# Optimization experiments

Measured on AMD Instinct MI355X. Metric: run time of the kernel, lower is better.

Reference implementation:

```python
import jax, jax.numpy as jnp
import numpy as np

B, A, N, FIN, H, HEADS, OUT = 32, 64, 121, 12, 128, 4, 256
NL = 2          # transformer encoder layers
LEVELS = 4      # complete ternary tree: N = (3**(LEVELS+1)-1)//2 = 121
EPS = 1e-5


def setup_inputs() -> dict:
    key = jax.random.key(0)
    ks = jax.random.split(key, 10)
    s = 0.02
    # adjacency: complete ternary tree, local node indices, rows [parent, child, branch]
    child = np.arange(1, N)
    parent = (child - 1) // 3
    branch = (child - 1) % 3
    adj = np.stack([parent, child, branch], -1).astype(np.int32)  # (N-1, 3)
    adjacency = jnp.asarray(np.broadcast_to(adj, (B, A, N - 1, 3)).copy())
    perm = jax.random.permutation(ks[0], N)  # torch.randperm(n_nodes) equivalent
    forest = jax.random.normal(ks[1], (B, A, N, FIN), jnp.float32)
    p = lambda k, shape: s * jax.random.normal(k, shape, jnp.float32)
    return dict(
        forest=forest, adjacency=adjacency, perm=perm,
        w_in=p(ks[2], (H, FIN)), b_in=jnp.zeros((H,), jnp.float32),
        qkv_w=p(ks[3], (NL, 3 * H, H)), qkv_b=jnp.zeros((NL, 3 * H), jnp.float32),
        proj_w=p(ks[4], (NL, H, H)), proj_b=jnp.zeros((NL, H), jnp.float32),
        ff1_w=p(ks[5], (NL, H, H)), ff1_b=jnp.zeros((NL, H), jnp.float32),
        ff2_w=p(ks[6], (NL, H, H)), ff2_b=jnp.zeros((NL, H), jnp.float32),
        ln1_g=jnp.ones((NL, H), jnp.float32), ln1_b=jnp.zeros((NL, H), jnp.float32),
        ln2_g=jnp.ones((NL, H), jnp.float32), ln2_b=jnp.zeros((NL, H), jnp.float32),
        w_out=p(ks[7], (OUT, N * H)), b_out=jnp.zeros((OUT,), jnp.float32),
        lnf_g=jnp.ones((OUT,), jnp.float32), lnf_b=jnp.zeros((OUT,), jnp.float32))


def _ln(x, g, b):
    m = x.mean(-1, keepdims=True)
    v = ((x - m) ** 2).mean(-1, keepdims=True)  # biased var, as torch LayerNorm
    return (x - m) * jax.lax.rsqrt(v + EPS) * g + b


def _tree_pe(adjacency):
    """Level-parallel tree positional encoding: pe[child] = pe[parent] with
    bit (depth*3 + branch) set to 1 (depth 0 = first level below root)."""
    parent = adjacency[..., 0]
    branch = adjacency[..., 2]
    pe = jnp.zeros((B, A, N, H), jnp.float32)
    for l in range(1, LEVELS + 1):
        s0 = (3 ** l - 1) // 2          # first node index at level l
        e0 = (3 ** (l + 1) - 1) // 2    # one past last node at level l
        pa = parent[..., s0 - 1:e0 - 1]             # (B, A, n_l) parent local idx
        br = branch[..., s0 - 1:e0 - 1]             # (B, A, n_l) branch 0/1/2
        ppe = jnp.take_along_axis(pe, pa[..., None], axis=2)  # gather parent PE
        bits = jax.nn.one_hot((l - 1) * 3 + br, H, dtype=jnp.float32)
        pe = pe.at[:, :, s0:e0, :].set(ppe + bits)
    return pe


def _mha(x, wqkv, bqkv, wo, bo):
    S = x.shape[0]
    hd = H // HEADS
    qkv = x @ wqkv.T + bqkv
    q, k, v = [t.reshape(S, N, HEADS, hd) for t in jnp.split(qkv, 3, axis=-1)]
    logits = jnp.einsum('bqhd,bkhd->bhqk', q, k) / float(np.sqrt(hd))
    o = jnp.einsum('bhqk,bkhd->bqhd', jax.nn.softmax(logits, -1), v)
    return o.reshape(S, N, H) @ wo.T + bo


def _forward(forest, adjacency, perm, w_in, b_in, qkv_w, qkv_b, proj_w, proj_b,
             ff1_w, ff1_b, ff2_w, ff2_b, ln1_g, ln1_b, ln2_g, ln2_b,
             w_out, b_out, lnf_g, lnf_b):
    x = forest @ w_in.T + b_in + _tree_pe(adjacency)        # (B, A, N, H)
    x = x.reshape(B * A, N, H)[:, perm]                      # token shuffle
    for i in range(NL):  # post-norm encoder layers, relu FFN, dropout=0
        x = _ln(x + _mha(x, qkv_w[i], qkv_b[i], proj_w[i], proj_b[i]), ln1_g[i], ln1_b[i])
        h = jnp.maximum(x @ ff1_w[i].T + ff1_b[i], 0.0)
        x = _ln(x + h @ ff2_w[i].T + ff2_b[i], ln2_g[i], ln2_b[i])
    y = x.reshape(B * A, N * H) @ w_out.T + b_out
    return _ln(y.reshape(B, A, OUT), lnf_g, lnf_b)


def reference(forest, adjacency, perm, w_in, b_in, qkv_w, qkv_b, proj_w, proj_b,
              ff1_w, ff1_b, ff2_w, ff2_b, ln1_g, ln1_b, ln2_g, ln2_b,
              w_out, b_out, lnf_g, lnf_b):
    return _forward(forest, adjacency, perm, w_in, b_in, qkv_w, qkv_b, proj_w, proj_b,
                    ff1_w, ff1_b, ff2_w, ff2_b, ln1_g, ln1_b, ln2_g, ln2_b,
                    w_out, b_out, lnf_g, lnf_b)
```

## Files before the change

kernel.cpp:

```cpp
#include <hip/hip_runtime.h>


typedef unsigned short u16;
typedef __attribute__((ext_vector_type(8))) short bf16x8;
typedef __attribute__((ext_vector_type(4))) float f32x4;
typedef __attribute__((ext_vector_type(4))) unsigned int u32x4;
typedef __attribute__((ext_vector_type(2))) unsigned int u32x2;

#define NTOK 121
#define HD 128
#define S_TOT 2048
#define EPSF 1e-5f

__device__ inline u16 f2bf(float f) {
  unsigned u = __float_as_uint(f);
  return (u16)((u + 0x7FFFu + ((u >> 16) & 1u)) >> 16);
}
__device__ inline float bf2f(u16 h) { return __uint_as_float(((unsigned)h) << 16); }
__device__ inline float bfu32lo(unsigned u) { return __uint_as_float(u << 16); }
__device__ inline float bfu32hi(unsigned u) { return __uint_as_float(u & 0xffff0000u); }

__device__ inline f32x4 mfma16(bf16x8 a, bf16x8 b, f32x4 c) {
  return __builtin_amdgcn_mfma_f32_16x16x32_bf16(a, b, c, 0, 0, 0);
}

__device__ inline unsigned cvt_pk_bf16(float lo, float hi) {
  unsigned r;
  asm("v_cvt_pk_bf16_f32 %0, %1, %2" : "=v"(r) : "v"(lo), "v"(hi));
  return r;
}

__device__ inline f32x4 vmax4(f32x4 a, f32x4 b) {
  f32x4 r;
  r[0] = fmaxf(a[0], b[0]); r[1] = fmaxf(a[1], b[1]);
  r[2] = fmaxf(a[2], b[2]); r[3] = fmaxf(a[3], b[3]);
  return r;
}

__device__ inline void stage16(const void* g, void* l) {
  __builtin_amdgcn_global_load_lds((__attribute__((address_space(1))) void*)g,
                                   (__attribute__((address_space(3))) void*)l,
                                   16, 0, 0);
}

__device__ inline void quad_repack(unsigned pkA, unsigned pkB, int quad,
                                   unsigned& mlo, unsigned& mhi) {
  unsigned y = (quad < 2) ? pkA : pkB;
  unsigned z = (quad < 2) ? pkB : pkA;
  unsigned a16 = (unsigned)__shfl_xor((int)y, 16);
  unsigned a32 = (unsigned)__shfl_xor((int)z, 32);
  unsigned a48 = (unsigned)__shfl_xor((int)z, 48);
  mlo = (quad == 0) ? y   : (quad == 1) ? a48 : (quad == 2) ? a32 : a16;
  mhi = (quad == 0) ? a16 : (quad == 1) ? a32 : (quad == 2) ? a48 : y;
}

__global__ __launch_bounds__(256) void convw_kernel(
    const float* __restrict__ qkvw, const float* __restrict__ projw,
    const float* __restrict__ ff1w, const float* __restrict__ ff2w,
    const float* __restrict__ wout, u16* __restrict__ dst) {
  int i = blockIdx.x * 256 + threadIdx.x;
  float v;
  if (i < 98304) v = qkvw[i];
  else if (i < 131072) v = projw[i - 98304];
  else if (i < 163840) v = ff1w[i - 131072];
  else if (i < 196608) v = ff2w[i - 163840];
  else v = wout[i - 196608];
  dst[i] = f2bf(v);
}

__global__ __launch_bounds__(256) void inproj_kernel(
    const float* __restrict__ forest, const int* __restrict__ adj,
    const int* __restrict__ perm, const float* __restrict__ WIN,
    const float* __restrict__ BIN, u16* __restrict__ X) {
  __shared__ float wf[128 * 12];
  __shared__ float fr[121 * 12];
  __shared__ float pe[121 * 12];
  __shared__ int pm[121];
  int s = blockIdx.x, tid = threadIdx.x;
  const float* fg = forest + (size_t)s * (NTOK * 12);
  const int* ag = adj + (size_t)s * (120 * 3);
  for (int i = tid; i < 128 * 12; i += 256) wf[i] = WIN[i];
  for (int i = tid; i < 121 * 12; i += 256) { fr[i] = fg[i]; pe[i] = 0.f; }
  if (tid < 121) pm[tid] = perm[tid];
  __syncthreads();
  if (tid > 0 && tid < 121) {
    int n = tid;
    int l = (n <= 3) ? 1 : (n <= 12) ? 2 : (n <= 39) ? 3 : 4;
    int cur = n;
    while (cur > 0) {
      int par = ag[(cur - 1) * 3];
      int br = ag[(cur - 1) * 3 + 2];
      pe[n * 12 + (l - 1) * 3 + br] = 1.f;
      cur = par; l--;
    }
  }
  __syncthreads();
  int h = tid & 127;
  for (int base = 0; base < 121; base += 2) {
    int i = base + (tid >> 7);
    if (i < 121) {
      int node = pm[i];
      float v = BIN[h];
#pragma unroll
      for (int k = 0; k < 12; ++k) v += fr[node * 12 + k] * wf[h * 12 + k];
      if (h < 12) v += pe[node * 12 + h];
      X[(size_t)s * (NTOK * HD) + i * HD + h] = f2bf(v);
    }
  }
}

__global__ __launch_bounds__(256, 3) void attn_kernel(
    const u16* __restrict__ X, u16* __restrict__ O,
    const u16* __restrict__ WQKV, const float* __restrict__ QKVB, int layer) {
  __shared__ u16 lds[8192];
  __shared__ u16 xl[15872];
  int tid = threadIdx.x;
  int wave = tid >> 6, lane = tid & 63, l16 = lane & 15, quad = lane >> 4;
  int seq = blockIdx.x >> 2;
  int head = blockIdx.x & 3;
  u16* Kh = lds;
  u16* Vh = lds + 4096;
  const u16* Xs = X + (size_t)seq * (NTOK * HD);
  const f32x4 fz = {0.f, 0.f, 0.f, 0.f};
  const int wbase = layer * 384 + head * 32;
  const u16* WQ = WQKV + (size_t)wbase * HD;
  const u16* WK = WQKV + (size_t)(wbase + 128) * HD;
  const u16* WV = WQKV + (size_t)(wbase + 256) * HD;

  {
    const char* Xb = (const char*)Xs;
#pragma unroll
    for (int j = 0; j < 8; ++j) {
      int i = wave * 8 + j;
      if (i < 31) {
        int n = i * 64 + lane;
        int r = n >> 4, c = n & 15;
        int rc = r > 120 ? 120 : r;
        stage16(Xb + rc * 256 + ((c ^ (r & 7)) << 4), (void*)(xl + i * 512));
      }
    }
  }
  bf16x8 wqf[2][4], wkf[2][4], wvf[2][4];
#pragma unroll
  for (int nt = 0; nt < 2; ++nt)
#pragma unroll
    for (int k = 0; k < 4; ++k) {
      size_t off = (size_t)(nt * 16 + l16) * HD + k * 32 + quad * 8;
      wqf[nt][k] = *(const bf16x8*)(WQ + off);
      wkf[nt][k] = *(const bf16x8*)(WK + off);
      wvf[nt][k] = *(const bf16x8*)(WV + off);
    }
  float kb2[2], vb2[2];
#pragma unroll
  for (int nt = 0; nt < 2; ++nt) {
    kb2[nt] = QKVB[wbase + 128 + nt * 16 + l16];
    vb2[nt] = QKVB[wbase + 256 + nt * 16 + l16];
  }
  const float scl = 0.17677669529663687f * 1.4426950408889634f;
  float qbias[2][4];
#pragma unroll
  for (int nt = 0; nt < 2; ++nt)
#pragma unroll
    for (int r = 0; r < 4; ++r)
      qbias[nt][r] = QKVB[wbase + nt * 16 + quad * 4 + r];
  asm volatile("s_waitcnt vmcnt(0)" ::: "memory");
  __syncthreads();

#pragma unroll 1
  for (int mt = 0; mt < 2; ++mt) {
    int tb = wave * 32 + mt * 16;
    int arow = tb + l16; if (arow > 120) arow = 120;
    bf16x8 a[4];
#pragma unroll
    for (int k = 0; k < 4; ++k)
      a[k] = *(const bf16x8*)(xl + arow * 128 + (((k * 4 + quad) ^ (arow & 7)) << 3));
#pragma unroll
    for (int nt = 0; nt < 2; ++nt) {
      f32x4 kacc = fz, vacc = fz;
      __builtin_amdgcn_s_setprio(1);
#pragma unroll
      for (int k = 0; k < 4; ++k) {
        kacc = mfma16(a[k], wkf[nt][k], kacc);
        vacc = mfma16(a[k], wvf[nt][k], vacc);
      }
      __builtin_amdgcn_s_setprio(0);
      int d = nt * 16 + l16;
      int kc = nt * 2 + (l16 >> 3);
#pragma unroll
      for (int r = 0; r < 4; ++r) {
        int t = tb + quad * 4 + r;
        Kh[t * 32 + ((kc ^ (t & 3)) << 3) + (l16 & 7)] = f2bf(kacc[r] + kb2[nt]);
      }
      float vv[4];
#pragma unroll
      for (int r = 0; r < 4; ++r) {
        int t = tb + quad * 4 + r;
        vv[r] = (t < NTOK) ? (vacc[r] + vb2[nt]) : 0.f;
      }
      u32x2 vp = { cvt_pk_bf16(vv[0], vv[1]), cvt_pk_bf16(vv[2], vv[3]) };
      *(u32x2*)(Vh + d * 128 + ((((tb >> 3) + (quad >> 1)) ^ l16) << 3) + (quad & 1) * 4) = vp;
    }
  }
  __syncthreads();

#pragma unroll 1
  for (int qmt = 0; qmt < 2; ++qmt) {
    int qb = wave * 32 + qmt * 16;
    int qrow = qb + l16;
    int qrowc = qrow > 120 ? 120 : qrow;
    bf16x8 xb[4];
#pragma unroll
    for (int k = 0; k < 4; ++k)
      xb[k] = *(const bf16x8*)(xl + qrowc * 128 + (((k * 4 + quad) ^ (qrowc & 7)) << 3));
    f32x4 qv[2];
    __builtin_amdgcn_s_setprio(1);
#pragma unroll
    for (int nt = 0; nt < 2; ++nt) {
      f32x4 acc = fz;
#pragma unroll
      for (int k = 0; k < 4; ++k) acc = mfma16(wqf[nt][k], xb[k], acc);
      qv[nt] = acc;
    }
    __builtin_amdgcn_s_setprio(0);
    unsigned qpk[2][2];
#pragma unroll
    for (int nt = 0; nt < 2; ++nt)
#pragma unroll
      for (int r2 = 0; r2 < 2; ++r2)
        qpk[nt][r2] = cvt_pk_bf16((qv[nt][2 * r2] + qbias[nt][2 * r2]) * scl,
                                  (qv[nt][2 * r2 + 1] + qbias[nt][2 * r2 + 1]) * scl);
    u32x4 qu;
#pragma unroll
    for (int r2 = 0; r2 < 2; ++r2) {
      unsigned mlo, mhi;
      quad_repack(qpk[0][r2], qpk[1][r2], quad, mlo, mhi);
      qu[r2] = mlo; qu[2 + r2] = mhi;
    }
    bf16x8 qfrag = __builtin_bit_cast(bf16x8, qu);
    f32x4 lg[8];
    __builtin_amdgcn_s_setprio(1);
#pragma unroll
    for (int nt = 0; nt < 8; ++nt) {
      bf16x8 ka = *(const bf16x8*)(Kh + (nt * 16 + l16) * 32 + ((quad ^ (l16 & 3)) << 3));
      lg[nt] = mfma16(ka, qfrag, fz);
    }
    __builtin_amdgcn_s_setprio(0);
    f32x4 t0 = vmax4(vmax4(lg[0], lg[1]), vmax4(lg[2], lg[3]));
    f32x4 t1 = vmax4(vmax4(lg[4], lg[5]), vmax4(lg[6], lg[7]));
    f32x4 tm = vmax4(t0, t1);
    float mx = fmaxf(fmaxf(tm[0], tm[1]), fmaxf(tm[2], tm[3]));
    mx = fmaxf(mx, __shfl_xor(mx, 16));
    mx = fmaxf(mx, __shfl_xor(mx, 32));
#pragma unroll
    for (int nt = 0; nt < 8; ++nt)
#pragma unroll
      for (int r = 0; r < 4; ++r) {
        float ev = __builtin_amdgcn_exp2f(lg[nt][r] - mx);
        if (nt == 7 && (quad * 4 + r > 8)) ev = 0.f;
        lg[nt][r] = ev;
      }
    f32x4 s4 = (lg[0] + lg[1]) + (lg[2] + lg[3]) + ((lg[4] + lg[5]) + (lg[6] + lg[7]));
    float sum = (s4[0] + s4[1]) + (s4[2] + s4[3]);
    sum += __shfl_xor(sum, 16);
    sum += __shfl_xor(sum, 32);
    float rinv = __builtin_amdgcn_rcpf(sum);
    unsigned pk[8][2];
#pragma unroll
    for (int nt = 0; nt < 8; ++nt)
#pragma unroll
      for (int r2 = 0; r2 < 2; ++r2)
        pk[nt][r2] = cvt_pk_bf16(lg[nt][2 * r2], lg[nt][2 * r2 + 1]);
    f32x4 oacc[2] = {fz, fz};
#pragma unroll
    for (int s = 0; s < 4; ++s) {
      u32x4 pu;
#pragma unroll
      for (int r2 = 0; r2 < 2; ++r2) {
        unsigned mlo, mhi;
        quad_repack(pk[2 * s][r2], pk[2 * s + 1][r2], quad, mlo, mhi);
        pu[r2] = mlo; pu[2 + r2] = mhi;
      }
      bf16x8 pfrag = __builtin_bit_cast(bf16x8, pu);
      __builtin_amdgcn_s_setprio(1);
#pragma unroll
      for (int mt = 0; mt < 2; ++mt) {
        bf16x8 va = *(const bf16x8*)(Vh + (mt * 16 + l16) * 128 + (((s * 4 + quad) ^ l16) << 3));
        oacc[mt] = mfma16(va, pfrag, oacc[mt]);
      }
      __builtin_amdgcn_s_setprio(0);
    }
    if (qrow < NTOK) {
      u16* Op = O + (size_t)seq * (NTOK * HD) + (size_t)qrow * HD + head * 32;
#pragma unroll
      for (int mt = 0; mt < 2; ++mt) {
        u32x2 w = { cvt_pk_bf16(oacc[mt][0] * rinv, oacc[mt][1] * rinv),
                    cvt_pk_bf16(oacc[mt][2] * rinv, oacc[mt][3] * rinv) };
        *(u32x2*)(Op + mt * 16 + quad * 4) = w;
      }
    }
  }
}

__global__ __launch_bounds__(256, 2) void blockln_kernel(
    u16* __restrict__ X, const u16* __restrict__ O,
    const u16* __restrict__ WP, const float* __restrict__ PB,
    const u16* __restrict__ W1, const float* __restrict__ B1,
    const u16* __restrict__ W2, const float* __restrict__ B2,
    const float* __restrict__ G1, const float* __restrict__ Bt1,
    const float* __restrict__ G2, const float* __restrict__ Bt2, int layer) {
  __shared__ u16 as_[128 * 128];
  __shared__ u16 xr[128 * 128];
  __shared__ float part[1024];
  int r0 = blockIdx.x * 128, tid = threadIdx.x;
  int wave = tid >> 6, lane = tid & 63, l16 = lane & 15, quad = lane >> 4;
  const f32x4 fz = {0.f, 0.f, 0.f, 0.f};
  const int Lb = layer * 128;
  const int ch0 = wave * 32;
  const int ch8b = wave * 4 + (quad >> 1);

  {
    const char* Ob = (const char*)(O + (size_t)r0 * HD);
    const char* Xb = (const char*)(X + (size_t)r0 * HD);
#pragma unroll
    for (int j = 0; j < 8; ++j) {
      int n = wave * 512 + j * 64 + lane;
      int r = n >> 4, c = n & 15;
      int gsrc = r * 256 + ((c ^ (r & 7)) << 4);
      stage16(Ob + gsrc, (void*)(as_ + (wave * 512 + j * 64) * 8));
      stage16(Xb + gsrc, (void*)(xr + (wave * 512 + j * 64) * 8));
    }
  }
  bf16x8 wpf[2][4], w1f[2][4], w2f[2][4];
#pragma unroll
  for (int g = 0; g < 2; ++g)
#pragma unroll
    for (int k = 0; k < 4; ++k) {
      size_t off = (size_t)(Lb + ch0 + g * 16 + l16) * HD + k * 32 + quad * 8;
      wpf[g][k] = *(const bf16x8*)(WP + off);
      w1f[g][k] = *(const bf16x8*)(W1 + off);
      w2f[g][k] = *(const bf16x8*)(W2 + off);
    }
  asm volatile("s_waitcnt vmcnt(0)" ::: "memory");
  __syncthreads();

  f32x4 acc[2][8];
#pragma unroll
  for (int mt = 0; mt < 8; ++mt) {
    int tok = mt * 16 + l16;
    bf16x8 of[4];
#pragma unroll
    for (int k = 0; k < 4; ++k)
      of[k] = *(const bf16x8*)(as_ + tok * 128 + (((k * 4 + quad) ^ (tok & 7)) << 3));
    __builtin_amdgcn_s_setprio(1);
#pragma unroll
    for (int g = 0; g < 2; ++g) {
      f32x4 a = fz;
#pragma unroll
      for (int k = 0; k < 4; ++k) a = mfma16(wpf[g][k], of[k], a);
      acc[g][mt] = a;
    }
    __builtin_amdgcn_s_setprio(0);
    float sum = 0.f, ssq = 0.f;
#pragma unroll
    for (int g = 0; g < 2; ++g) {
      float4 pb4 = *(const float4*)(PB + Lb + ch0 + g * 16 + quad * 4);
      int sl = (ch8b + g * 2) ^ (tok & 7);
      u32x2 xw = *(const u32x2*)(xr + tok * 128 + (sl << 3) + (quad & 1) * 4);
      acc[g][mt][0] += pb4.x + bfu32lo(xw[0]);
      acc[g][mt][1] += pb4.y + bfu32hi(xw[0]);
      acc[g][mt][2] += pb4.z + bfu32lo(xw[1]);
      acc[g][mt][3] += pb4.w + bfu32hi(xw[1]);
#pragma unroll
      for (int r = 0; r < 4; ++r) { sum += acc[g][mt][r]; ssq += acc[g][mt][r] * acc[g][mt][r]; }
    }
    sum += __shfl_xor(sum, 16); ssq += __shfl_xor(ssq, 16);
    sum += __shfl_xor(sum, 32); ssq += __shfl_xor(ssq, 32);
    if (quad == 0) *(float2*)(part + ((mt * 4 + wave) * 16 + l16) * 2) = make_float2(sum, ssq);
  }
  __syncthreads();

#pragma unroll
  for (int mt = 0; mt < 8; ++mt) {
    int tok = mt * 16 + l16;
    float sum = 0.f, ssq = 0.f;
#pragma unroll
    for (int ww = 0; ww < 4; ++ww) {
      float2 p = *(const float2*)(part + ((mt * 4 + ww) * 16 + l16) * 2);
      sum += p.x; ssq += p.y;
    }
    float mean = sum * (1.f / 128.f);
    float rstd = rsqrtf(ssq * (1.f / 128.f) - mean * mean + EPSF);
#pragma unroll
    for (int g = 0; g < 2; ++g) {
      float4 g4 = *(const float4*)(G1 + Lb + ch0 + g * 16 + quad * 4);
      float4 b4 = *(const float4*)(Bt1 + Lb + ch0 + g * 16 + quad * 4);
      u32x2 wv = { cvt_pk_bf16((acc[g][mt][0] - mean) * rstd * g4.x + b4.x,
                               (acc[g][mt][1] - mean) * rstd * g4.y + b4.y),
                   cvt_pk_bf16((acc[g][mt][2] - mean) * rstd * g4.z + b4.z,
                               (acc[g][mt][3] - mean) * rstd * g4.w + b4.w) };
      int sl = (ch8b + g * 2) ^ (tok & 7);
      *(u32x2*)(as_ + tok * 128 + (sl << 3) + (quad & 1) * 4) = wv;
    }
  }
  __syncthreads();

#pragma unroll
  for (int mt = 0; mt < 8; ++mt) {
    int tok = mt * 16 + l16;
    bf16x8 af[4];
#pragma unroll
    for (int k = 0; k < 4; ++k)
      af[k] = *(const bf16x8*)(as_ + tok * 128 + (((k * 4 + quad) ^ (tok & 7)) << 3));
    __builtin_amdgcn_s_setprio(1);
#pragma unroll
    for (int g = 0; g < 2; ++g) {
      f32x4 a = fz;
#pragma unroll
      for (int k = 0; k < 4; ++k) a = mfma16(w1f[g][k], af[k], a);
      float4 b14 = *(const float4*)(B1 + Lb + ch0 + g * 16 + quad * 4);
      u32x2 wv = { cvt_pk_bf16(fmaxf(a[0] + b14.x, 0.f), fmaxf(a[1] + b14.y, 0.f)),
                   cvt_pk_bf16(fmaxf(a[2] + b14.z, 0.f), fmaxf(a[3] + b14.w, 0.f)) };
      int sl = (ch8b + g * 2) ^ (tok & 7);
      *(u32x2*)(xr + tok * 128 + (sl << 3) + (quad & 1) * 4) = wv;
    }
    __builtin_amdgcn_s_setprio(0);
  }
  __syncthreads();

#pragma unroll
  for (int mt = 0; mt < 8; ++mt) {
    int tok = mt * 16 + l16;
    bf16x8 hf[4];
#pragma unroll
    for (int k = 0; k < 4; ++k)
      hf[k] = *(const bf16x8*)(xr + tok * 128 + (((k * 4 + quad) ^ (tok & 7)) << 3));
    __builtin_amdgcn_s_setprio(1);
#pragma unroll
    for (int g = 0; g < 2; ++g) {
      f32x4 a = fz;
#pragma unroll
      for (int k = 0; k < 4; ++k) a = mfma16(w2f[g][k], hf[k], a);
      acc[g][mt] = a;
    }
    __builtin_amdgcn_s_setprio(0);
    float sum = 0.f, ssq = 0.f;
#pragma unroll
    for (int g = 0; g < 2; ++g) {
      float4 b24 = *(const float4*)(B2 + Lb + ch0 + g * 16 + quad * 4);
      int sl = (ch8b + g * 2) ^ (tok & 7);
      u32x2 lw = *(const u32x2*)(as_ + tok * 128 + (sl << 3) + (quad & 1) * 4);
      acc[g][mt][0] += b24.x + bfu32lo(lw[0]);
      acc[g][mt][1] += b24.y + bfu32hi(lw[0]);
      acc[g][mt][2] += b24.z + bfu32lo(lw[1]);
      acc[g][mt][3] += b24.w + bfu32hi(lw[1]);
#pragma unroll
      for (int r = 0; r < 4; ++r) { sum += acc[g][mt][r]; ssq += acc[g][mt][r] * acc[g][mt][r]; }
    }
    sum += __shfl_xor(sum, 16); ssq += __shfl_xor(ssq, 16);
    sum += __shfl_xor(sum, 32); ssq += __shfl_xor(ssq, 32);
    if (quad == 0) *(float2*)(part + ((mt * 4 + wave) * 16 + l16) * 2) = make_float2(sum, ssq);
  }
  __syncthreads();

#pragma unroll
  for (int mt = 0; mt < 8; ++mt) {
    int tok = mt * 16 + l16;
    float sum = 0.f, ssq = 0.f;
#pragma unroll
    for (int ww = 0; ww < 4; ++ww) {
      float2 p = *(const float2*)(part + ((mt * 4 + ww) * 16 + l16) * 2);
      sum += p.x; ssq += p.y;
    }
    float mean = sum * (1.f / 128.f);
    float rstd = rsqrtf(ssq * (1.f / 128.f) - mean * mean + EPSF);
    u16* Xp = X + (size_t)(r0 + tok) * HD + ch0;
#pragma unroll
    for (int g = 0; g < 2; ++g) {
      float4 g4 = *(const float4*)(G2 + Lb + ch0 + g * 16 + quad * 4);
      float4 b4 = *(const float4*)(Bt2 + Lb + ch0 + g * 16 + quad * 4);
      u32x2 wv = { cvt_pk_bf16((acc[g][mt][0] - mean) * rstd * g4.x + b4.x,
                               (acc[g][mt][1] - mean) * rstd * g4.y + b4.y),
                   cvt_pk_bf16((acc[g][mt][2] - mean) * rstd * g4.z + b4.z,
                               (acc[g][mt][3] - mean) * rstd * g4.w + b4.w) };
      *(u32x2*)(Xp + g * 16 + quad * 4) = wv;
    }
  }
}

__global__ __launch_bounds__(256, 2) void outgemm_kernel(
    const u16* __restrict__ X, const u16* __restrict__ WO, float* __restrict__ PART) {
  __shared__ u16 as_[64 * 136];
  int mtile = blockIdx.x, j = blockIdx.y;
  int tid = threadIdx.x, wave = tid >> 6, lane = tid & 63, l16 = lane & 15, quad = lane >> 4;
  int s0 = mtile * 64;
  int k0 = (j * 484) / 16, k1 = ((j + 1) * 484) / 16;
  const f32x4 fz = {0.f, 0.f, 0.f, 0.f};
  f32x4 acc[4][4];
  for (int a = 0; a < 4; ++a) for (int b = 0; b < 4; ++b) acc[a][b] = fz;
  for (int kb = k0; kb < k1; kb += 4) {
    int nst = (k1 - kb < 4) ? (k1 - kb) : 4;
    __syncthreads();
    int chunks = 64 * 4 * nst;
    for (int c = tid; c < chunks; c += 256) {
      int row = c / (4 * nst), g = c % (4 * nst);
      *(uint4*)(as_ + row * 136 + g * 8) =
          *(const uint4*)(X + (size_t)(s0 + row) * 15488 + kb * 32 + g * 8);
    }
    __syncthreads();
    for (int kk = 0; kk < nst; ++kk) {
      bf16x8 af[4];
#pragma unroll
      for (int mt = 0; mt < 4; ++mt)
        af[mt] = *(const bf16x8*)(as_ + (mt * 16 + l16) * 136 + kk * 32 + quad * 8);
#pragma unroll
      for (int n = 0; n < 4; ++n) {
        int nt = wave * 4 + n;
        bf16x8 bf = *(const bf16x8*)(WO + (size_t)(nt * 16 + l16) * 15488 +
                                     (size_t)(kb + kk) * 32 + quad * 8);
#pragma unroll
        for (int mt = 0; mt < 4; ++mt) acc[mt][n] = mfma16(af[mt], bf, acc[mt][n]);
      }
    }
  }
  for (int mt = 0; mt < 4; ++mt)
    for (int n = 0; n < 4; ++n) {
      int nt = wave * 4 + n;
#pragma unroll
      for (int r = 0; r < 4; ++r) {
        int row = s0 + mt * 16 + quad * 4 + r;
        PART[((size_t)j * 2048 + row) * 256 + nt * 16 + l16] = acc[mt][n][r];
      }
    }
}

__global__ __launch_bounds__(256) void lnf_kernel(
    const float* __restrict__ PART, const float* __restrict__ BO,
    const float* __restrict__ G, const float* __restrict__ Bt, float* __restrict__ OUT) {
  int s = blockIdx.x * 4 + (threadIdx.x >> 6);
  int lane = threadIdx.x & 63;
  float v[4], sum = 0.f, ssq = 0.f;
#pragma unroll
  for (int i = 0; i < 4; ++i) {
    int c = lane + i * 64;
    float t = BO[c];
    for (int jj = 0; jj < 16; ++jj) t += PART[((size_t)jj * 2048 + s) * 256 + c];
    v[i] = t; sum += t; ssq += t * t;
  }
  for (int m = 1; m <= 32; m <<= 1) { sum += __shfl_xor(sum, m, 64); ssq += __shfl_xor(ssq, m, 64); }
  float mean = sum * (1.f / 256.f);
  float var = ssq * (1.f / 256.f) - mean * mean;
  float rstd = rsqrtf(var + EPSF);
#pragma unroll
  for (int i = 0; i < 4; ++i) {
    int c = lane + i * 64;
    OUT[(size_t)s * 256 + c] = (v[i] - mean) * rstd * G[c] + Bt[c];
  }
}

extern "C" void kernel_launch(void* const* d_in, const int* in_sizes, int n_in,
                              void* d_out, int out_size, void* d_ws, size_t ws_size,
                              hipStream_t stream) {
  const float* forest = (const float*)d_in[0];
  const int* adj      = (const int*)d_in[1];
  const int* perm     = (const int*)d_in[2];
  const float* w_in   = (const float*)d_in[3];
  const float* b_in   = (const float*)d_in[4];
  const float* qkv_w  = (const float*)d_in[5];
  const float* qkv_b  = (const float*)d_in[6];
  const float* proj_w = (const float*)d_in[7];
  const float* proj_b = (const float*)d_in[8];
  const float* ff1_w  = (const float*)d_in[9];
  const float* ff1_b  = (const float*)d_in[10];
  const float* ff2_w  = (const float*)d_in[11];
  const float* ff2_b  = (const float*)d_in[12];
  const float* ln1_g  = (const float*)d_in[13];
  const float* ln1_b  = (const float*)d_in[14];
  const float* ln2_g  = (const float*)d_in[15];
  const float* ln2_b  = (const float*)d_in[16];
  const float* w_out  = (const float*)d_in[17];
  const float* b_out  = (const float*)d_in[18];
  const float* lnf_g  = (const float*)d_in[19];
  const float* lnf_b  = (const float*)d_in[20];

  char* ws = (char*)d_ws;
  u16* WB = (u16*)ws;
  u16* X  = (u16*)(ws + 8323072);
  u16* O  = (u16*)(ws + 8323072 + 63438848);
  float* PART = (float*)(ws + 8323072 + 2 * (size_t)63438848);

  u16* WQKV  = WB;
  u16* WPROJ = WB + 98304;
  u16* WFF1  = WB + 131072;
  u16* WFF2  = WB + 163840;
  u16* WOUT  = WB + 196608;

  convw_kernel<<<16256, 256, 0, stream>>>(qkv_w, proj_w, ff1_w, ff2_w, w_out, WB);
  inproj_kernel<<<2048, 256, 0, stream>>>(forest, adj, perm, w_in, b_in, X);
  for (int layer = 0; layer < 2; ++layer) {
    attn_kernel<<<8192, 256, 0, stream>>>(X, O, WQKV, qkv_b, layer);
    blockln_kernel<<<1936, 256, 0, stream>>>(X, O, WPROJ, proj_b, WFF1, ff1_b,
                                             WFF2, ff2_b, ln1_g, ln1_b, ln2_g, ln2_b, layer);
  }
  outgemm_kernel<<<dim3(32, 16), 256, 0, stream>>>(X, WOUT, PART);
  lnf_kernel<<<512, 256, 0, stream>>>(PART, b_out, lnf_g, lnf_b, (float*)d_out);
}
```

Measured before the change: 610.7 us.

## Process two attention heads per block to reuse staged sequence tile

Each attention block now handles two heads of one sequence, not one, so the grid is halved. The sequence's X tile is staged into LDS once and reused for both heads. This halves the global X reads and the staging overhead. In exchange each block does serial work for two heads, with a reload of the per-head weights and an extra barrier between them, and there are fewer blocks to hide latency.

```diff
diff --git a/kernel.cpp b/kernel.cpp
--- a/kernel.cpp
+++ b/kernel.cpp
@@ -109,6 +109,26 @@
   }
 }
 
+#define LOADW()                                                              \
+  do {                                                                       \
+    const u16* WQ = WQKV + (size_t)wbase * HD;                               \
+    const u16* WK = WQKV + (size_t)(wbase + 128) * HD;                       \
+    const u16* WV = WQKV + (size_t)(wbase + 256) * HD;                       \
+    _Pragma("unroll") for (int nt = 0; nt < 2; ++nt)                         \
+        _Pragma("unroll") for (int k = 0; k < 4; ++k) {                      \
+      size_t off = (size_t)(nt * 16 + l16) * HD + k * 32 + quad * 8;         \
+      wqf[nt][k] = *(const bf16x8*)(WQ + off);                               \
+      wkf[nt][k] = *(const bf16x8*)(WK + off);                               \
+      wvf[nt][k] = *(const bf16x8*)(WV + off);                               \
+    }                                                                        \
+    _Pragma("unroll") for (int nt = 0; nt < 2; ++nt) {                       \
+      kb2[nt] = QKVB[wbase + 128 + nt * 16 + l16];                           \
+      vb2[nt] = QKVB[wbase + 256 + nt * 16 + l16];                           \
+      _Pragma("unroll") for (int r = 0; r < 4; ++r)                          \
+          qbias[nt][r] = QKVB[wbase + nt * 16 + quad * 4 + r];               \
+    }                                                                        \
+  } while (0)
+
 __global__ __launch_bounds__(256, 3) void attn_kernel(
     const u16* __restrict__ X, u16* __restrict__ O,
     const u16* __restrict__ WQKV, const float* __restrict__ QKVB, int layer) {
@@ -116,16 +136,13 @@
   __shared__ u16 xl[15872];
   int tid = threadIdx.x;
   int wave = tid >> 6, lane = tid & 63, l16 = lane & 15, quad = lane >> 4;
-  int seq = blockIdx.x >> 2;
-  int head = blockIdx.x & 3;
+  int seq = blockIdx.x >> 1;
+  int hb = (blockIdx.x & 1) << 1;
   u16* Kh = lds;
   u16* Vh = lds + 4096;
   const u16* Xs = X + (size_t)seq * (NTOK * HD);
   const f32x4 fz = {0.f, 0.f, 0.f, 0.f};
-  const int wbase = layer * 384 + head * 32;
-  const u16* WQ = WQKV + (size_t)wbase * HD;
-  const u16* WK = WQKV + (size_t)(wbase + 128) * HD;
-  const u16* WV = WQKV + (size_t)(wbase + 256) * HD;
+  const float scl = 0.17677669529663687f * 1.4426950408889634f;
 
   {
     const char* Xb = (const char*)Xs;
@@ -141,163 +158,154 @@
     }
   }
   bf16x8 wqf[2][4], wkf[2][4], wvf[2][4];
-#pragma unroll
-  for (int nt = 0; nt < 2; ++nt)
-#pragma unroll
-    for (int k = 0; k < 4; ++k) {
-      size_t off = (size_t)(nt * 16 + l16) * HD + k * 32 + quad * 8;
-      wqf[nt][k] = *(const bf16x8*)(WQ + off);
-      wkf[nt][k] = *(const bf16x8*)(WK + off);
-      wvf[nt][k] = *(const bf16x8*)(WV + off);
-    }
-  float kb2[2], vb2[2];
-#pragma unroll
-  for (int nt = 0; nt < 2; ++nt) {
-    kb2[nt] = QKVB[wbase + 128 + nt * 16 + l16];
-    vb2[nt] = QKVB[wbase + 256 + nt * 16 + l16];
-  }
-  const float scl = 0.17677669529663687f * 1.4426950408889634f;
-  float qbias[2][4];
-#pragma unroll
-  for (int nt = 0; nt < 2; ++nt)
-#pragma unroll
-    for (int r = 0; r < 4; ++r)
-      qbias[nt][r] = QKVB[wbase + nt * 16 + quad * 4 + r];
+  float kb2[2], vb2[2], qbias[2][4];
+  int wbase = layer * 384 + hb * 32;
+  LOADW();
   asm volatile("s_waitcnt vmcnt(0)" ::: "memory");
   __syncthreads();
 
 #pragma unroll 1
-  for (int mt = 0; mt < 2; ++mt) {
-    int tb = wave * 32 + mt * 16;
-    int arow = tb + l16; if (arow > 120) arow = 120;
-    bf16x8 a[4];
-#pragma unroll
-    for (int k = 0; k < 4; ++k)
-      a[k] = *(const bf16x8*)(xl + arow * 128 + (((k * 4 + quad) ^ (arow & 7)) << 3));
-#pragma unroll
-    for (int nt = 0; nt < 2; ++nt) {
-      f32x4 kacc = fz, vacc = fz;
+  for (int hp = 0; hp < 2; ++hp) {
+    if (hp) {
+      wbase = layer * 384 + (hb + 1) * 32;
+      LOADW();
+    }
+    int head = hb + hp;
+
+#pragma unroll 1
+    for (int mt = 0; mt < 2; ++mt) {
+      int tb = wave * 32 + mt * 16;
+      int arow = tb + l16; if (arow > 120) arow = 120;
+      bf16x8 a[4];
+#pragma unroll
+      for (int k = 0; k < 4; ++k)
+        a[k] = *(const bf16x8*)(xl + arow * 128 + (((k * 4 + quad) ^ (arow & 7)) << 3));
+#pragma unroll
+      for (int nt = 0; nt < 2; ++nt) {
+        f32x4 kacc = fz, vacc = fz;
+        __builtin_amdgcn_s_setprio(1);
+#pragma unroll
+        for (int k = 0; k < 4; ++k) {
+          kacc = mfma16(a[k], wkf[nt][k], kacc);
+          vacc = mfma16(a[k], wvf[nt][k], vacc);
+        }
+        __builtin_amdgcn_s_setprio(0);
+        int d = nt * 16 + l16;
+        int kc = nt * 2 + (l16 >> 3);
+#pragma unroll
+        for (int r = 0; r < 4; ++r) {
+          int t = tb + quad * 4 + r;
+          Kh[t * 32 + ((kc ^ (t & 3)) << 3) + (l16 & 7)] = f2bf(kacc[r] + kb2[nt]);
+        }
+        float vv[4];
+#pragma unroll
+        for (int r = 0; r < 4; ++r) {
+          int t = tb + quad * 4 + r;
+          vv[r] = (t < NTOK) ? (vacc[r] + vb2[nt]) : 0.f;
+        }
+        u32x2 vp = { cvt_pk_bf16(vv[0], vv[1]), cvt_pk_bf16(vv[2], vv[3]) };
+        *(u32x2*)(Vh + d * 128 + ((((tb >> 3) + (quad >> 1)) ^ l16) << 3) + (quad & 1) * 4) = vp;
+      }
+    }
+    __syncthreads();
+
+#pragma unroll 1
+    for (int qmt = 0; qmt < 2; ++qmt) {
+      int qb = wave * 32 + qmt * 16;
+      int qrow = qb + l16;
+      int qrowc = qrow > 120 ? 120 : qrow;
+      bf16x8 xb[4];
+#pragma unroll
+      for (int k = 0; k < 4; ++k)
+        xb[k] = *(const bf16x8*)(xl + qrowc * 128 + (((k * 4 + quad) ^ (qrowc & 7)) << 3));
+      f32x4 qv[2];
       __builtin_amdgcn_s_setprio(1);
 #pragma unroll
-      for (int k = 0; k < 4; ++k) {
-        kacc = mfma16(a[k], wkf[nt][k], kacc);
-        vacc = mfma16(a[k], wvf[nt][k], vacc);
+      for (int nt = 0; nt < 2; ++nt) {
+        f32x4 acc = fz;
+#pragma unroll
+        for (int k = 0; k < 4; ++k) acc = mfma16(wqf[nt][k], xb[k], acc);
+        qv[nt] = acc;
       }
       __builtin_amdgcn_s_setprio(0);
-      int d = nt * 16 + l16;
-      int kc = nt * 2 + (l16 >> 3);
-#pragma unroll
-      for (int r = 0; r < 4; ++r) {
-        int t = tb + quad * 4 + r;
-        Kh[t * 32 + ((kc ^ (t & 3)) << 3) + (l16 & 7)] = f2bf(kacc[r] + kb2[nt]);
-      }
-      float vv[4];
-#pragma unroll
-      for (int r = 0; r < 4; ++r) {
-        int t = tb + quad * 4 + r;
-        vv[r] = (t < NTOK) ? (vacc[r] + vb2[nt]) : 0.f;
-      }
-      u32x2 vp = { cvt_pk_bf16(vv[0], vv[1]), cvt_pk_bf16(vv[2], vv[3]) };
-      *(u32x2*)(Vh + d * 128 + ((((tb >> 3) + (quad >> 1)) ^ l16) << 3) + (quad & 1) * 4) = vp;
-    }
-  }
-  __syncthreads();
-
-#pragma unroll 1
-  for (int qmt = 0; qmt < 2; ++qmt) {
-    int qb = wave * 32 + qmt * 16;
-    int qrow = qb + l16;
-    int qrowc = qrow > 120 ? 120 : qrow;
-    bf16x8 xb[4];
-#pragma unroll
-    for (int k = 0; k < 4; ++k)
-      xb[k] = *(const bf16x8*)(xl + qrowc * 128 + (((k * 4 + quad) ^ (qrowc & 7)) << 3));
-    f32x4 qv[2];
-    __builtin_amdgcn_s_setprio(1);
-#pragma unroll
-    for (int nt = 0; nt < 2; ++nt) {
-      f32x4 acc = fz;
-#pragma unroll
-      for (int k = 0; k < 4; ++k) acc = mfma16(wqf[nt][k], xb[k], acc);
-      qv[nt] = acc;
-    }
-    __builtin_amdgcn_s_setprio(0);
-    unsigned qpk[2][2];
-#pragma unroll
-    for (int nt = 0; nt < 2; ++nt)
-#pragma unroll
-      for (int r2 = 0; r2 < 2; ++r2)
-        qpk[nt][r2] = cvt_pk_bf16((qv[nt][2 * r2] + qbias[nt][2 * r2]) * scl,
-                                  (qv[nt][2 * r2 + 1] + qbias[nt][2 * r2 + 1]) * scl);
-    u32x4 qu;
-#pragma unroll
-    for (int r2 = 0; r2 < 2; ++r2) {
-      unsigned mlo, mhi;
-      quad_repack(qpk[0][r2], qpk[1][r2], quad, mlo, mhi);
-      qu[r2] = mlo; qu[2 + r2] = mhi;
-    }
-    bf16x8 qfrag = __builtin_bit_cast(bf16x8, qu);
-    f32x4 lg[8];
-    __builtin_amdgcn_s_setprio(1);
-#pragma unroll
-    for (int nt = 0; nt < 8; ++nt) {
-      bf16x8 ka = *(const bf16x8*)(Kh + (nt * 16 + l16) * 32 + ((quad ^ (l16 & 3)) << 3));
-      lg[nt] = mfma16(ka, qfrag, fz);
-    }
-    __builtin_amdgcn_s_setprio(0);
-    f32x4 t0 = vmax4(vmax4(lg[0], lg[1]), vmax4(lg[2], lg[3]));
-    f32x4 t1 = vmax4(vmax4(lg[4], lg[5]), vmax4(lg[6], lg[7]));
-    f32x4 tm = vmax4(t0, t1);
-    float mx = fmaxf(fmaxf(tm[0], tm[1]), fmaxf(tm[2], tm[3]));
-    mx = fmaxf(mx, __shfl_xor(mx, 16));
-    mx = fmaxf(mx, __shfl_xor(mx, 32));
-#pragma unroll
-    for (int nt = 0; nt < 8; ++nt)
-#pragma unroll
-      for (int r = 0; r < 4; ++r) {
-        float ev = __builtin_amdgcn_exp2f(lg[nt][r] - mx);
-        if (nt == 7 && (quad * 4 + r > 8)) ev = 0.f;
-        lg[nt][r] = ev;
-      }
-    f32x4 s4 = (lg[0] + lg[1]) + (lg[2] + lg[3]) + ((lg[4] + lg[5]) + (lg[6] + lg[7]));
-    float sum = (s4[0] + s4[1]) + (s4[2] + s4[3]);
-    sum += __shfl_xor(sum, 16);
-    sum += __shfl_xor(sum, 32);
-    float rinv = __builtin_amdgcn_rcpf(sum);
-    unsigned pk[8][2];
-#pragma unroll
-    for (int nt = 0; nt < 8; ++nt)
-#pragma unroll
-      for (int r2 = 0; r2 < 2; ++r2)
-        pk[nt][r2] = cvt_pk_bf16(lg[nt][2 * r2], lg[nt][2 * r2 + 1]);
-    f32x4 oacc[2] = {fz, fz};
-#pragma unroll
-    for (int s = 0; s < 4; ++s) {
-      u32x4 pu;
+      unsigned qpk[2][2];
+#pragma unroll
+      for (int nt = 0; nt < 2; ++nt)
+#pragma unroll
+        for (int r2 = 0; r2 < 2; ++r2)
+          qpk[nt][r2] = cvt_pk_bf16((qv[nt][2 * r2] + qbias[nt][2 * r2]) * scl,
+                                    (qv[nt][2 * r2 + 1] + qbias[nt][2 * r2 + 1]) * scl);
+      u32x4 qu;
 #pragma unroll
       for (int r2 = 0; r2 < 2; ++r2) {
         unsigned mlo, mhi;
-        quad_repack(pk[2 * s][r2], pk[2 * s + 1][r2], quad, mlo, mhi);
-        pu[r2] = mlo; pu[2 + r2] = mhi;
-      }
-      bf16x8 pfrag = __builtin_bit_cast(bf16x8, pu);
+        quad_repack(qpk[0][r2], qpk[1][r2], quad, mlo, mhi);
+        qu[r2] = mlo; qu[2 + r2] = mhi;
+      }
+      bf16x8 qfrag = __builtin_bit_cast(bf16x8, qu);
+      f32x4 lg[8];
       __builtin_amdgcn_s_setprio(1);
 #pragma unroll
-      for (int mt = 0; mt < 2; ++mt) {
-        bf16x8 va = *(const bf16x8*)(Vh + (mt * 16 + l16) * 128 + (((s * 4 + quad) ^ l16) << 3));
-        oacc[mt] = mfma16(va, pfrag, oacc[mt]);
+      for (int nt = 0; nt < 8; ++nt) {
+        bf16x8 ka = *(const bf16x8*)(Kh + (nt * 16 + l16) * 32 + ((quad ^ (l16 & 3)) << 3));
+        lg[nt] = mfma16(ka, qfrag, fz);
       }
       __builtin_amdgcn_s_setprio(0);
-    }
-    if (qrow < NTOK) {
-      u16* Op = O + (size_t)seq * (NTOK * HD) + (size_t)qrow * HD + head * 32;
-#pragma unroll
-      for (int mt = 0; mt < 2; ++mt) {
-        u32x2 w = { cvt_pk_bf16(oacc[mt][0] * rinv, oacc[mt][1] * rinv),
-                    cvt_pk_bf16(oacc[mt][2] * rinv, oacc[mt][3] * rinv) };
-        *(u32x2*)(Op + mt * 16 + quad * 4) = w;
-      }
-    }
+      f32x4 t0 = vmax4(vmax4(lg[0], lg[1]), vmax4(lg[2], lg[3]));
+      f32x4 t1 = vmax4(vmax4(lg[4], lg[5]), vmax4(lg[6], lg[7]));
+      f32x4 tm = vmax4(t0, t1);
+      float mx = fmaxf(fmaxf(tm[0], tm[1]), fmaxf(tm[2], tm[3]));
+      mx = fmaxf(mx, __shfl_xor(mx, 16));
+      mx = fmaxf(mx, __shfl_xor(mx, 32));
+#pragma unroll
+      for (int nt = 0; nt < 8; ++nt)
+#pragma unroll
+        for (int r = 0; r < 4; ++r) {
+          float ev = __builtin_amdgcn_exp2f(lg[nt][r] - mx);
+          if (nt == 7 && (quad * 4 + r > 8)) ev = 0.f;
+          lg[nt][r] = ev;
+        }
+      f32x4 s4 = (lg[0] + lg[1]) + (lg[2] + lg[3]) + ((lg[4] + lg[5]) + (lg[6] + lg[7]));
+      float sum = (s4[0] + s4[1]) + (s4[2] + s4[3]);
+      sum += __shfl_xor(sum, 16);
+      sum += __shfl_xor(sum, 32);
+      float rinv = __builtin_amdgcn_rcpf(sum);
+      unsigned pk[8][2];
+#pragma unroll
+      for (int nt = 0; nt < 8; ++nt)
+#pragma unroll
+        for (int r2 = 0; r2 < 2; ++r2)
+          pk[nt][r2] = cvt_pk_bf16(lg[nt][2 * r2], lg[nt][2 * r2 + 1]);
+      f32x4 oacc[2] = {fz, fz};
+#pragma unroll
+      for (int s = 0; s < 4; ++s) {
+        u32x4 pu;
+#pragma unroll
+        for (int r2 = 0; r2 < 2; ++r2) {
+          unsigned mlo, mhi;
+          quad_repack(pk[2 * s][r2], pk[2 * s + 1][r2], quad, mlo, mhi);
+          pu[r2] = mlo; pu[2 + r2] = mhi;
+        }
+        bf16x8 pfrag = __builtin_bit_cast(bf16x8, pu);
+        __builtin_amdgcn_s_setprio(1);
+#pragma unroll
+        for (int mt = 0; mt < 2; ++mt) {
+          bf16x8 va = *(const bf16x8*)(Vh + (mt * 16 + l16) * 128 + (((s * 4 + quad) ^ l16) << 3));
+          oacc[mt] = mfma16(va, pfrag, oacc[mt]);
+        }
+        __builtin_amdgcn_s_setprio(0);
+      }
+      if (qrow < NTOK) {
+        u16* Op = O + (size_t)seq * (NTOK * HD) + (size_t)qrow * HD + head * 32;
+#pragma unroll
+        for (int mt = 0; mt < 2; ++mt) {
+          u32x2 w = { cvt_pk_bf16(oacc[mt][0] * rinv, oacc[mt][1] * rinv),
+                      cvt_pk_bf16(oacc[mt][2] * rinv, oacc[mt][3] * rinv) };
+          *(u32x2*)(Op + mt * 16 + quad * 4) = w;
+        }
+      }
+    }
+    if (hp == 0) __syncthreads();
   }
 }
 
@@ -597,7 +605,7 @@
   convw_kernel<<<16256, 256, 0, stream>>>(qkv_w, proj_w, ff1_w, ff2_w, w_out, WB);
   inproj_kernel<<<2048, 256, 0, stream>>>(forest, adj, perm, w_in, b_in, X);
   for (int layer = 0; layer < 2; ++layer) {
-    attn_kernel<<<8192, 256, 0, stream>>>(X, O, WQKV, qkv_b, layer);
+    attn_kernel<<<4096, 256, 0, stream>>>(X, O, WQKV, qkv_b, layer);
     blockln_kernel<<<1936, 256, 0, stream>>>(X, O, WPROJ, proj_b, WFF1, ff1_b,
                                              WFF2, ff2_b, ln1_g, ln1_b, ln2_g, ln2_b, layer);
   }
```

Measured after the change: 767.2 us. 1.26x slower.
